# Kernel tuning notes

Hardware: AMD Instinct MI355X
Metric: run time of the kernel (lower is better)

Reference implementation:

```python
import jax, jax.numpy as jnp
import numpy as np

B, S, D, H = 4, 1024, 1024, 16
HD = D // H


def setup_inputs() -> dict:
    key = jax.random.key(0)
    ks = jax.random.split(key, 8)
    x = jax.random.normal(ks[0], (B, S, D), dtype=jnp.float32)
    attn_bias = jax.random.normal(ks[1], (B, H, S, S), dtype=jnp.float32) * 0.1
    pos_ids = jnp.broadcast_to(jnp.arange(S, dtype=jnp.int32), (B, S))
    lengths = jnp.array([S, S - 64, S - 128, S - 256], dtype=jnp.int32)
    pad_mask = jnp.arange(S)[None, :] >= lengths[:, None]  # True = padded key
    scale = 0.02
    Wq = jax.random.normal(ks[2], (D, D), dtype=jnp.float32) * scale
    Wk = jax.random.normal(ks[3], (D, D), dtype=jnp.float32) * scale
    Wv = jax.random.normal(ks[4], (D, D), dtype=jnp.float32) * scale
    Wo = jax.random.normal(ks[5], (D, D), dtype=jnp.float32) * scale
    bq = jnp.zeros((D,), jnp.float32); bk = jnp.zeros((D,), jnp.float32)
    bv = jnp.zeros((D,), jnp.float32); bo = jnp.zeros((D,), jnp.float32)
    return {"x": x, "attn_bias": attn_bias, "pos_ids": pos_ids, "pad_mask": pad_mask,
            "Wq": Wq, "bq": bq, "Wk": Wk, "bk": bk, "Wv": Wv, "bv": bv, "Wo": Wo, "bo": bo}


def _apply_rotary(q, k, pos_ids):
    # q,k: [B,S,H,HD]; pos_ids: [B,S]
    hd = q.shape[-1]
    inv_freq = 1.0 / (10000.0 ** (jnp.arange(0, hd, 2, dtype=jnp.float32) / hd))
    freqs = pos_ids.astype(jnp.float32)[:, :, None] * inv_freq  # [B,S,HD/2]
    emb = jnp.concatenate([freqs, freqs], axis=-1)[:, :, None, :]  # [B,S,1,HD]
    cos, sin = jnp.cos(emb), jnp.sin(emb)
    def rot_half(t):
        t1, t2 = jnp.split(t, 2, axis=-1)
        return jnp.concatenate([-t2, t1], axis=-1)
    return q * cos + rot_half(q) * sin, k * cos + rot_half(k) * sin


def reference(x, attn_bias, pos_ids, pad_mask, Wq, bq, Wk, bk, Wv, bv, Wo, bo):
    b, s, d = x.shape
    q = (x @ Wq.T + bq).reshape(b, s, H, HD)
    k = (x @ Wk.T + bk).reshape(b, s, H, HD)
    v = (x @ Wv.T + bv).reshape(b, s, H, HD)
    q, k = _apply_rotary(q, k, pos_ids)
    q = q.transpose(0, 2, 1, 3)  # [B,H,S,HD]
    k = k.transpose(0, 2, 1, 3)
    v = v.transpose(0, 2, 1, 3)
    scores = jnp.einsum("bhqd,bhkd->bhqk", q, k) / np.sqrt(HD).astype(np.float32)
    scores = scores + attn_bias
    scores = jnp.where(pad_mask[:, None, None, :], -jnp.inf, scores)
    attn = jax.nn.softmax(scores, axis=-1)  # dropout p=0 -> identity
    out = jnp.einsum("bhqk,bhkd->bqhd", attn, v).reshape(b, s, d)
    metric = k.mean(axis=1)  # mean over heads -> [B,S,HD]
    return out @ Wo.T + bo, metric
```

## Files before the change

### kernel.cpp

```cpp
#include <hip/hip_runtime.h>
#include <hip/hip_bf16.h>

#define SS 1024
#define DD 1024
#define HH 16
#define HDD 64

using f32x4  = __attribute__((ext_vector_type(4))) float;
using bf16x8 = __attribute__((ext_vector_type(8))) __bf16;
using bf16x4 = __attribute__((ext_vector_type(4))) __bf16;

__device__ __forceinline__ void gload_lds16(const void* g, void* l) {
  __builtin_amdgcn_global_load_lds((__attribute__((address_space(1))) void*)g,
                                   (__attribute__((address_space(3))) void*)l, 16, 0, 0);
}

__global__ void convert_kernel(const float4* __restrict__ x, const float4* __restrict__ Wq,
                               const float4* __restrict__ Wk, const float4* __restrict__ Wv,
                               const float4* __restrict__ Wo,
                               bf16x4* __restrict__ xb, bf16x4* __restrict__ wqkvb,
                               bf16x4* __restrict__ wob, float4* __restrict__ metric) {
  int i = blockIdx.x * 256 + threadIdx.x;
  if (blockIdx.x < 256) {
    float4 z = {0.f, 0.f, 0.f, 0.f};
    metric[blockIdx.x * 256 + threadIdx.x] = z;
  }
  float4 v; bf16x4* dst;
  if (i < 1048576)      { v = x[i];              dst = xb + i; }
  else if (i < 1310720) { v = Wq[i - 1048576];   dst = wqkvb + (i - 1048576); }
  else if (i < 1572864) { v = Wk[i - 1310720];   dst = wqkvb + 262144 + (i - 1310720); }
  else if (i < 1835008) { v = Wv[i - 1572864];   dst = wqkvb + 524288 + (i - 1572864); }
  else                  { v = Wo[i - 1835008];   dst = wob + (i - 1835008); }
  bf16x4 o;
  o[0] = (__bf16)v.x; o[1] = (__bf16)v.y; o[2] = (__bf16)v.z; o[3] = (__bf16)v.w;
  *dst = o;
}

template<int EPI>
__global__ __launch_bounds__(256, 2)
void gemm_kernel(const __bf16* __restrict__ A, const __bf16* __restrict__ Bm, int N,
                 const float* __restrict__ b0, const float* __restrict__ b1,
                 const float* __restrict__ b2, const int* __restrict__ pos_ids,
                 __bf16* __restrict__ Qr, __bf16* __restrict__ Kr, __bf16* __restrict__ Vtg,
                 float* __restrict__ metric, float* __restrict__ Cout) {
  __shared__ __align__(16) char smem[17408];
  __bf16* As = (__bf16*)smem;
  __bf16* Bs = (__bf16*)(smem + 8192);
  const int tid = threadIdx.x;
  const int wid = tid >> 6, lane = tid & 63;
  const int g = lane >> 4, cl = lane & 15;
  const int ntn = N >> 7;
  const int bm = blockIdx.x / ntn, bn = blockIdx.x % ntn;
  const int m0 = bm << 7, n0 = bn << 7;
  const int wr = (wid >> 1) << 6, wc = (wid & 1) << 6;

  f32x4 acc[4][4] = {};

  for (int kk = 0; kk < 1024; kk += 32) {
    __syncthreads();
#pragma unroll
    for (int p = 0; p < 2; ++p) {
      int idx = p * 256 + tid;
      gload_lds16(A  + (size_t)(m0 + (idx >> 2)) * 1024 + kk + ((idx & 3) << 3),
                  (char*)As + p * 4096 + wid * 1024);
      gload_lds16(Bm + (size_t)(n0 + (idx >> 2)) * 1024 + kk + ((idx & 3) << 3),
                  (char*)Bs + p * 4096 + wid * 1024);
    }
    __syncthreads();
    bf16x8 fa[4], fb[4];
#pragma unroll
    for (int i = 0; i < 4; ++i)
      fa[i] = *(const bf16x8*)(As + (wr + i * 16 + cl) * 32 + g * 8);
#pragma unroll
    for (int j = 0; j < 4; ++j)
      fb[j] = *(const bf16x8*)(Bs + (wc + j * 16 + cl) * 32 + g * 8);
#pragma unroll
    for (int i = 0; i < 4; ++i)
#pragma unroll
      for (int j = 0; j < 4; ++j)
        acc[i][j] = __builtin_amdgcn_mfma_f32_16x16x32_bf16(fa[i], fb[j], acc[i][j], 0, 0, 0);
  }

  if constexpr (EPI == 1) {
#pragma unroll
    for (int j = 0; j < 4; ++j) {
      int col = n0 + wc + j * 16 + cl;
      float bv = b0[col];
#pragma unroll
      for (int i = 0; i < 4; ++i)
#pragma unroll
        for (int r = 0; r < 4; ++r) {
          int row = m0 + wr + i * 16 + g * 4 + r;
          Cout[(size_t)row * 1024 + col] = acc[i][j][r] + bv;
        }
    }
  } else if (n0 >= 2048) {
    __bf16* vt_s = (__bf16*)smem;
    const int b_ = m0 >> 10, s0 = m0 & 1023;
    const int vbase = n0 - 2048;
#pragma unroll
    for (int phase = 0; phase < 2; ++phase) {
      __syncthreads();
      if ((wid & 1) == phase) {
#pragma unroll
        for (int j = 0; j < 4; ++j) {
          int d = j * 16 + cl;
          float bv = b2[vbase + wc + d];
#pragma unroll
          for (int i = 0; i < 4; ++i)
#pragma unroll
            for (int r = 0; r < 4; ++r)
              vt_s[d * 136 + wr + i * 16 + g * 4 + r] = (__bf16)(acc[i][j][r] + bv);
        }
      }
      __syncthreads();
      int hh = (vbase >> 6) + phase;
#pragma unroll
      for (int p = 0; p < 4; ++p) {
        int d = p * 16 + (tid >> 4), s8 = (tid & 15) * 8;
        bf16x8 v = *(const bf16x8*)(vt_s + d * 136 + s8);
        *(bf16x8*)(Vtg + ((size_t)(b_ * HH + hh) * HDD + d) * SS + s0 + s8) = v;
      }
    }
  } else {
    const int cb = n0 + wc;
    const int region = cb >> 10;
    const int hcol = (cb & 1023) >> 6;
    const int cir = cb & 1023;
    const float* bias = region == 0 ? b0 : b1;
    __bf16* dst = region == 0 ? Qr : Kr;
    float invf0 = exp2f(-0.4152410118609203f * (float)(cl));
    float invf1 = exp2f(-0.4152410118609203f * (float)(16 + cl));
#pragma unroll
    for (int i = 0; i < 4; ++i) {
#pragma unroll
      for (int r = 0; r < 4; ++r) {
        int row = m0 + wr + i * 16 + g * 4 + r;
        int b_ = row >> 10, s = row & 1023;
        size_t ob = ((size_t)(b_ * HH + hcol) * SS + s) * HDD;
        float pos = (float)pos_ids[row];
#pragma unroll
        for (int j = 0; j < 2; ++j) {
          int dlo = j * 16 + cl;
          float vlo = acc[i][j][r]     + bias[cir + dlo];
          float vhi = acc[i][j + 2][r] + bias[cir + dlo + 32];
          float th = pos * (j == 0 ? invf0 : invf1);
          float sn, cs;
          __sincosf(th, &sn, &cs);
          float olo = vlo * cs - vhi * sn;
          float ohi = vhi * cs + vlo * sn;
          dst[ob + dlo]      = (__bf16)olo;
          dst[ob + dlo + 32] = (__bf16)ohi;
          if (region == 1) {
            atomicAdd(&metric[(size_t)row * HDD + dlo],      olo * 0.0625f);
            atomicAdd(&metric[(size_t)row * HDD + dlo + 32], ohi * 0.0625f);
          }
        }
      }
    }
  }
}

__global__ __launch_bounds__(512, 4)
void attn_kernel(const __bf16* __restrict__ Qr, const __bf16* __restrict__ Kr,
                 const __bf16* __restrict__ Vtg, const float* __restrict__ bias,
                 const int* __restrict__ pad, __bf16* __restrict__ attn_out) {
  __shared__ __align__(16) __bf16 Ks[2][64][64];
  __shared__ __align__(16) __bf16 Vt[2][64][64];
  __shared__ __align__(16) __bf16 Plds[8][16][68];
  const int tid = threadIdx.x;
  const int wid = tid >> 6, lane = tid & 63;
  const int g = lane >> 4, cl = lane & 15;
  const int bh = blockIdx.x & 63, b_ = bh >> 4, h = bh & 15;
  const int q0 = (blockIdx.x >> 6) * 128 + wid * 16;
  const __bf16* Qb = Qr  + ((size_t)bh << 16);
  const __bf16* Kb = Kr  + ((size_t)bh << 16);
  const __bf16* Vb = Vtg + ((size_t)bh << 16);
  const float*  Bb = bias + ((size_t)bh << 20);
  const int* padb = pad + b_ * SS;

  int pm = (lane < 16) ? padb[lane * 64] : 1;
  unsigned long long ball = __ballot(pm == 0);
  const int ntile = __popcll(ball & 0xFFFFull);

  const int l8 = lane >> 3, l7 = lane & 7;
  const int krow = 8 * wid + l8;
  const int kchk = l7 ^ l8;
  const int swz = cl & 7;

  gload_lds16(Kb + (size_t)krow * 64 + kchk * 8, (char*)&Ks[0][8 * wid][0]);
  gload_lds16(Vb + (size_t)krow * SS + kchk * 8, (char*)&Vt[0][8 * wid][0]);
  float breg[4][4];
#pragma unroll
  for (int kt = 0; kt < 4; ++kt)
#pragma unroll
    for (int r = 0; r < 4; ++r)
      breg[kt][r] = Bb[(size_t)(q0 + 4 * g + r) * SS + kt * 16 + cl];

  bf16x8 aq0 = *(const bf16x8*)(Qb + (size_t)(q0 + cl) * 64 + g * 8);
  bf16x8 aq1 = *(const bf16x8*)(Qb + (size_t)(q0 + cl) * 64 + 32 + g * 8);
  bf16x8 onesb;
#pragma unroll
  for (int j = 0; j < 8; ++j) onesb[j] = (__bf16)1.0f;

  f32x4 o[4] = {};
  float m_l[4] = {-1e30f, -1e30f, -1e30f, -1e30f};
  float l_l[4] = {0.f, 0.f, 0.f, 0.f};

  for (int t = 0; t < ntile; ++t) {
    const int buf = t & 1;
    __syncthreads();
    if (t + 1 < ntile) {
      int kk = (t + 1) * 64;
      gload_lds16(Kb + (size_t)(kk + krow) * 64 + kchk * 8, (char*)&Ks[buf ^ 1][8 * wid][0]);
      gload_lds16(Vb + (size_t)krow * SS + kk + kchk * 8,   (char*)&Vt[buf ^ 1][8 * wid][0]);
    }

    f32x4 sc[4];
    __builtin_amdgcn_s_setprio(1);
#pragma unroll
    for (int kt = 0; kt < 4; ++kt) {
      bf16x8 kb0 = *(const bf16x8*)(&Ks[buf][kt * 16 + cl][(g ^ swz) * 8]);
      bf16x8 kb1 = *(const bf16x8*)(&Ks[buf][kt * 16 + cl][((g + 4) ^ swz) * 8]);
      f32x4 z = {0.f, 0.f, 0.f, 0.f};
      z = __builtin_amdgcn_mfma_f32_16x16x32_bf16(aq0, kb0, z, 0, 0, 0);
      sc[kt] = __builtin_amdgcn_mfma_f32_16x16x32_bf16(aq1, kb1, z, 0, 0, 0);
    }
    __builtin_amdgcn_s_setprio(0);

#pragma unroll
    for (int kt = 0; kt < 4; ++kt)
#pragma unroll
      for (int r = 0; r < 4; ++r)
        sc[kt][r] = sc[kt][r] * 0.125f + breg[kt][r];
    if (t + 1 < ntile) {
      int kk = (t + 1) * 64;
#pragma unroll
      for (int kt = 0; kt < 4; ++kt)
#pragma unroll
        for (int r = 0; r < 4; ++r)
          breg[kt][r] = Bb[(size_t)(q0 + 4 * g + r) * SS + kk + kt * 16 + cl];
    }

    float mx[4];
#pragma unroll
    for (int r = 0; r < 4; ++r)
      mx[r] = fmaxf(fmaxf(sc[0][r], sc[1][r]), fmaxf(sc[2][r], sc[3][r]));
#pragma unroll
    for (int d = 1; d < 16; d <<= 1)
#pragma unroll
      for (int r = 0; r < 4; ++r) mx[r] = fmaxf(mx[r], __shfl_xor(mx[r], d, 64));
    bool adv = true;
#pragma unroll
    for (int r = 0; r < 4; ++r) adv = adv && (mx[r] <= m_l[r] + 8.0f);
    if (!__all(adv)) {
#pragma unroll
      for (int r = 0; r < 4; ++r) {
        float nm = fmaxf(m_l[r], mx[r]);
        float s_ = __expf(m_l[r] - nm);
        m_l[r] = nm;
        l_l[r] *= s_;
#pragma unroll
        for (int dj = 0; dj < 4; ++dj) o[dj][r] *= s_;
      }
    }
#pragma unroll
    for (int kt = 0; kt < 4; ++kt)
#pragma unroll
      for (int r = 0; r < 4; ++r) sc[kt][r] = __expf(sc[kt][r] - m_l[r]);

#pragma unroll
    for (int kt = 0; kt < 4; ++kt)
#pragma unroll
      for (int r = 0; r < 4; ++r)
        Plds[wid][g * 4 + r][kt * 16 + cl] = (__bf16)sc[kt][r];
    bf16x8 pa0 = *(const bf16x8*)(&Plds[wid][cl][g * 8]);
    bf16x8 pa1 = *(const bf16x8*)(&Plds[wid][cl][32 + g * 8]);

    __builtin_amdgcn_s_setprio(1);
    f32x4 ls = {0.f, 0.f, 0.f, 0.f};
    ls = __builtin_amdgcn_mfma_f32_16x16x32_bf16(pa0, onesb, ls, 0, 0, 0);
    ls = __builtin_amdgcn_mfma_f32_16x16x32_bf16(pa1, onesb, ls, 0, 0, 0);
#pragma unroll
    for (int dj = 0; dj < 4; ++dj) {
      bf16x8 vb0 = *(const bf16x8*)(&Vt[buf][dj * 16 + cl][(g ^ swz) * 8]);
      bf16x8 vb1 = *(const bf16x8*)(&Vt[buf][dj * 16 + cl][((g + 4) ^ swz) * 8]);
      o[dj] = __builtin_amdgcn_mfma_f32_16x16x32_bf16(pa0, vb0, o[dj], 0, 0, 0);
      o[dj] = __builtin_amdgcn_mfma_f32_16x16x32_bf16(pa1, vb1, o[dj], 0, 0, 0);
    }
    __builtin_amdgcn_s_setprio(0);
#pragma unroll
    for (int r = 0; r < 4; ++r) l_l[r] += ls[r];
  }

#pragma unroll
  for (int dj = 0; dj < 4; ++dj)
#pragma unroll
    for (int r = 0; r < 4; ++r) {
      int qrow = q0 + g * 4 + r;
      attn_out[(size_t)(b_ * SS + qrow) * DD + h * 64 + dj * 16 + cl] =
          (__bf16)(o[dj][r] / l_l[r]);
    }
}

extern "C" void kernel_launch(void* const* d_in, const int* in_sizes, int n_in,
                              void* d_out, int out_size, void* d_ws, size_t ws_size,
                              hipStream_t stream) {
  const float* x  = (const float*)d_in[0];
  const float* ab = (const float*)d_in[1];
  const int* pos  = (const int*)d_in[2];
  const int* pad  = (const int*)d_in[3];
  const float* Wq = (const float*)d_in[4];
  const float* bq = (const float*)d_in[5];
  const float* Wk = (const float*)d_in[6];
  const float* bk = (const float*)d_in[7];
  const float* Wv = (const float*)d_in[8];
  const float* bv = (const float*)d_in[9];
  const float* Wo = (const float*)d_in[10];
  const float* bo = (const float*)d_in[11];
  float* out = (float*)d_out;
  float* metric = out + 4194304;

  char* ws = (char*)d_ws;
  __bf16* Qr   = (__bf16*)(ws);
  __bf16* Kr   = (__bf16*)(ws + 8388608);
  __bf16* Vtg  = (__bf16*)(ws + 16777216);
  __bf16* xb   = (__bf16*)(ws + 25165824);
  __bf16* wqkv = (__bf16*)(ws + 33554432);
  __bf16* wob  = (__bf16*)(ws + 39845888);
  __bf16* ao   = (__bf16*)(ws + 41943040);

  convert_kernel<<<8192, 256, 0, stream>>>((const float4*)x, (const float4*)Wq,
                                           (const float4*)Wk, (const float4*)Wv,
                                           (const float4*)Wo, (bf16x4*)xb,
                                           (bf16x4*)wqkv, (bf16x4*)wob, (float4*)metric);
  gemm_kernel<0><<<768, 256, 0, stream>>>(xb, wqkv, 3072, bq, bk, bv, pos,
                                          Qr, Kr, Vtg, metric, nullptr);
  attn_kernel<<<512, 512, 0, stream>>>(Qr, Kr, Vtg, ab, pad, ao);
  gemm_kernel<1><<<256, 256, 0, stream>>>(ao, wob, 1024, bo, nullptr, nullptr, nullptr,
                                          nullptr, nullptr, nullptr, nullptr, out);
}
```

Before: 170.7 us.

## Double-buffer GEMM with swizzled LDS, stage attention bias through LDS, retile attention

The GEMM now uses 64-wide K tiles with double-buffered, XOR-swizzled LDS staging and a single barrier per iteration. Its block index is remapped in an interleaved order, presumably for cache locality. The attention kernel now uses 256-thread blocks covering 64 queries each, with twice as many blocks, and brings the fp32 bias tile in through async global-to-LDS loads alongside K/V instead of per-thread register prefetch. This aims to hide global latency and reduce bank conflicts, at the cost of much more LDS per block (64KB in the GEMM), which can limit occupancy.

```diff
diff --git a/kernel.cpp b/kernel.cpp
--- a/kernel.cpp
+++ b/kernel.cpp
@@ -36,6 +36,20 @@
   *dst = o;
 }
 
+#define GEMM_STAGE(BUF, KK)                                                        \
+  {                                                                                \
+    char* Ab = smem + (BUF) * 32768;                                               \
+    char* Bb = Ab + 16384;                                                         \
+    _Pragma("unroll") for (int q = 0; q < 4; ++q) {                                \
+      int idx = q * 256 + tid;                                                     \
+      int row = idx >> 3, c = idx & 7;                                             \
+      gload_lds16(A  + (size_t)(m0 + row) * 1024 + (KK) + ((c ^ (row & 7)) << 3),  \
+                  Ab + q * 4096 + wid * 1024);                                     \
+      gload_lds16(Bm + (size_t)(n0 + row) * 1024 + (KK) + ((c ^ (row & 7)) << 3),  \
+                  Bb + q * 4096 + wid * 1024);                                     \
+    }                                                                              \
+  }
+
 template<int EPI>
 __global__ __launch_bounds__(256, 2)
 void gemm_kernel(const __bf16* __restrict__ A, const __bf16* __restrict__ Bm, int N,
@@ -43,42 +57,43 @@
                  const float* __restrict__ b2, const int* __restrict__ pos_ids,
                  __bf16* __restrict__ Qr, __bf16* __restrict__ Kr, __bf16* __restrict__ Vtg,
                  float* __restrict__ metric, float* __restrict__ Cout) {
-  __shared__ __align__(16) char smem[17408];
-  __bf16* As = (__bf16*)smem;
-  __bf16* Bs = (__bf16*)(smem + 8192);
+  __shared__ __align__(16) char smem[65536];
   const int tid = threadIdx.x;
   const int wid = tid >> 6, lane = tid & 63;
   const int g = lane >> 4, cl = lane & 15;
   const int ntn = N >> 7;
-  const int bm = blockIdx.x / ntn, bn = blockIdx.x % ntn;
+  const int tile = (blockIdx.x & 7) * ((int)gridDim.x >> 3) + (blockIdx.x >> 3);
+  const int bm = tile / ntn, bn = tile % ntn;
   const int m0 = bm << 7, n0 = bn << 7;
   const int wr = (wid >> 1) << 6, wc = (wid & 1) << 6;
+  const int swz = cl & 7;
 
   f32x4 acc[4][4] = {};
 
-  for (int kk = 0; kk < 1024; kk += 32) {
+  GEMM_STAGE(0, 0);
+  __syncthreads();
+  int buf = 0;
+  for (int t = 0; t < 16; ++t) {
+    if (t + 1 < 16) GEMM_STAGE(buf ^ 1, (t + 1) * 64);
+    const __bf16* Abuf = (const __bf16*)(smem + buf * 32768);
+    const __bf16* Bbuf = Abuf + 8192;
+#pragma unroll
+    for (int s = 0; s < 2; ++s) {
+      bf16x8 fa[4], fb[4];
+#pragma unroll
+      for (int i = 0; i < 4; ++i)
+        fa[i] = *(const bf16x8*)(Abuf + (wr + i * 16 + cl) * 64 + (((s * 4 + g) ^ swz) << 3));
+#pragma unroll
+      for (int j = 0; j < 4; ++j)
+        fb[j] = *(const bf16x8*)(Bbuf + (wc + j * 16 + cl) * 64 + (((s * 4 + g) ^ swz) << 3));
+#pragma unroll
+      for (int i = 0; i < 4; ++i)
+#pragma unroll
+        for (int j = 0; j < 4; ++j)
+          acc[i][j] = __builtin_amdgcn_mfma_f32_16x16x32_bf16(fa[i], fb[j], acc[i][j], 0, 0, 0);
+    }
     __syncthreads();
-#pragma unroll
-    for (int p = 0; p < 2; ++p) {
-      int idx = p * 256 + tid;
-      gload_lds16(A  + (size_t)(m0 + (idx >> 2)) * 1024 + kk + ((idx & 3) << 3),
-                  (char*)As + p * 4096 + wid * 1024);
-      gload_lds16(Bm + (size_t)(n0 + (idx >> 2)) * 1024 + kk + ((idx & 3) << 3),
-                  (char*)Bs + p * 4096 + wid * 1024);
-    }
-    __syncthreads();
-    bf16x8 fa[4], fb[4];
-#pragma unroll
-    for (int i = 0; i < 4; ++i)
-      fa[i] = *(const bf16x8*)(As + (wr + i * 16 + cl) * 32 + g * 8);
-#pragma unroll
-    for (int j = 0; j < 4; ++j)
-      fb[j] = *(const bf16x8*)(Bs + (wc + j * 16 + cl) * 32 + g * 8);
-#pragma unroll
-    for (int i = 0; i < 4; ++i)
-#pragma unroll
-      for (int j = 0; j < 4; ++j)
-        acc[i][j] = __builtin_amdgcn_mfma_f32_16x16x32_bf16(fa[i], fb[j], acc[i][j], 0, 0, 0);
+    buf ^= 1;
   }
 
   if constexpr (EPI == 1) {
@@ -161,18 +176,21 @@
   }
 }
 
-__global__ __launch_bounds__(512, 4)
+__global__ __launch_bounds__(256, 2)
 void attn_kernel(const __bf16* __restrict__ Qr, const __bf16* __restrict__ Kr,
                  const __bf16* __restrict__ Vtg, const float* __restrict__ bias,
                  const int* __restrict__ pad, __bf16* __restrict__ attn_out) {
+  __shared__ __align__(16) float  Bls[2][64][64];
   __shared__ __align__(16) __bf16 Ks[2][64][64];
   __shared__ __align__(16) __bf16 Vt[2][64][64];
-  __shared__ __align__(16) __bf16 Plds[8][16][68];
+  __shared__ __align__(16) __bf16 Plds[4][16][68];
   const int tid = threadIdx.x;
   const int wid = tid >> 6, lane = tid & 63;
   const int g = lane >> 4, cl = lane & 15;
   const int bh = blockIdx.x & 63, b_ = bh >> 4, h = bh & 15;
-  const int q0 = (blockIdx.x >> 6) * 128 + wid * 16;
+  const int qb = blockIdx.x >> 6;
+  const int q0 = qb * 64 + wid * 16;
+  const int q0b = qb * 64;
   const __bf16* Qb = Qr  + ((size_t)bh << 16);
   const __bf16* Kb = Kr  + ((size_t)bh << 16);
   const __bf16* Vb = Vtg + ((size_t)bh << 16);
@@ -184,19 +202,24 @@
   const int ntile = __popcll(ball & 0xFFFFull);
 
   const int l8 = lane >> 3, l7 = lane & 7;
-  const int krow = 8 * wid + l8;
   const int kchk = l7 ^ l8;
+  const int l16 = lane >> 4, lc = lane & 15;
   const int swz = cl & 7;
 
-  gload_lds16(Kb + (size_t)krow * 64 + kchk * 8, (char*)&Ks[0][8 * wid][0]);
-  gload_lds16(Vb + (size_t)krow * SS + kchk * 8, (char*)&Vt[0][8 * wid][0]);
-  float breg[4][4];
-#pragma unroll
-  for (int kt = 0; kt < 4; ++kt)
-#pragma unroll
-    for (int r = 0; r < 4; ++r)
-      breg[kt][r] = Bb[(size_t)(q0 + 4 * g + r) * SS + kt * 16 + cl];
-
+#define ATTN_STAGE(BUF, KK)                                                        \
+  {                                                                                \
+    _Pragma("unroll") for (int i_ = 0; i_ < 4; ++i_)                               \
+      gload_lds16(Bb + (size_t)(q0b + i_ * 16 + 4 * wid + l16) * SS + (KK) + lc * 4,\
+                  (char*)&Bls[BUF][i_ * 16 + 4 * wid][0]);                         \
+    _Pragma("unroll") for (int j_ = 0; j_ < 2; ++j_) {                             \
+      gload_lds16(Kb + (size_t)((KK) + j_ * 32 + 8 * wid + l8) * 64 + kchk * 8,    \
+                  (char*)&Ks[BUF][j_ * 32 + 8 * wid][0]);                          \
+      gload_lds16(Vb + (size_t)(j_ * 32 + 8 * wid + l8) * SS + (KK) + kchk * 8,    \
+                  (char*)&Vt[BUF][j_ * 32 + 8 * wid][0]);                          \
+    }                                                                              \
+  }
+
+  ATTN_STAGE(0, 0);
   bf16x8 aq0 = *(const bf16x8*)(Qb + (size_t)(q0 + cl) * 64 + g * 8);
   bf16x8 aq1 = *(const bf16x8*)(Qb + (size_t)(q0 + cl) * 64 + 32 + g * 8);
   bf16x8 onesb;
@@ -210,11 +233,14 @@
   for (int t = 0; t < ntile; ++t) {
     const int buf = t & 1;
     __syncthreads();
-    if (t + 1 < ntile) {
-      int kk = (t + 1) * 64;
-      gload_lds16(Kb + (size_t)(kk + krow) * 64 + kchk * 8, (char*)&Ks[buf ^ 1][8 * wid][0]);
-      gload_lds16(Vb + (size_t)krow * SS + kk + kchk * 8,   (char*)&Vt[buf ^ 1][8 * wid][0]);
-    }
+    if (t + 1 < ntile) ATTN_STAGE(buf ^ 1, (t + 1) * 64);
+
+    float bb[4][4];
+#pragma unroll
+    for (int kt = 0; kt < 4; ++kt)
+#pragma unroll
+      for (int r = 0; r < 4; ++r)
+        bb[kt][r] = Bls[buf][wid * 16 + 4 * g + r][kt * 16 + cl];
 
     f32x4 sc[4];
     __builtin_amdgcn_s_setprio(1);
@@ -227,20 +253,11 @@
       sc[kt] = __builtin_amdgcn_mfma_f32_16x16x32_bf16(aq1, kb1, z, 0, 0, 0);
     }
     __builtin_amdgcn_s_setprio(0);
-
 #pragma unroll
     for (int kt = 0; kt < 4; ++kt)
 #pragma unroll
       for (int r = 0; r < 4; ++r)
-        sc[kt][r] = sc[kt][r] * 0.125f + breg[kt][r];
-    if (t + 1 < ntile) {
-      int kk = (t + 1) * 64;
-#pragma unroll
-      for (int kt = 0; kt < 4; ++kt)
-#pragma unroll
-        for (int r = 0; r < 4; ++r)
-          breg[kt][r] = Bb[(size_t)(q0 + 4 * g + r) * SS + kk + kt * 16 + cl];
-    }
+        sc[kt][r] = sc[kt][r] * 0.125f + bb[kt][r];
 
     float mx[4];
 #pragma unroll
@@ -336,7 +353,7 @@
                                            (bf16x4*)wqkv, (bf16x4*)wob, (float4*)metric);
   gemm_kernel<0><<<768, 256, 0, stream>>>(xb, wqkv, 3072, bq, bk, bv, pos,
                                           Qr, Kr, Vtg, metric, nullptr);
-  attn_kernel<<<512, 512, 0, stream>>>(Qr, Kr, Vtg, ab, pad, ao);
+  attn_kernel<<<1024, 256, 0, stream>>>(Qr, Kr, Vtg, ab, pad, ao);
   gemm_kernel<1><<<256, 256, 0, stream>>>(ao, wob, 1024, bo, nullptr, nullptr, nullptr,
                                           nullptr, nullptr, nullptr, nullptr, out);
 }
```

Result: slower. 176.3 us (+3.2%).
